# Kernel tuning notes

Measured on AMD Instinct MI355X. Metric: run time of the kernel, lower is better.

Reference implementation:

```python
import jax, jax.numpy as jnp
import numpy as np


def _made_masks(D, H):
    # Standard MADE masks, natural ordering, param_count=2 (shift, log_scale).
    d_in = np.arange(1, D + 1)                      # input degrees 1..D
    d_h = (np.arange(H) % (D - 1)) + 1              # hidden degrees cycle 1..D-1
    d_out = np.tile(d_in, 2)                        # output degrees, 2 params per dim
    M1 = (d_h[None, :] >= d_in[:, None]).astype(np.float32)   # [D, H]
    M2 = (d_out[None, :] > d_h[:, None]).astype(np.float32)
    return jnp.asarray(M1), jnp.asarray(M2)


def setup_inputs() -> dict:
    key = jax.random.key(0)
    B, D, H = 4096, 1024, 4096
    k0, k1, k2 = jax.random.split(key, 3)
    z = jax.random.normal(k0, (B, D), dtype=jnp.float32)
    W1 = jax.random.normal(k1, (D, H), dtype=jnp.float32) * (1.0 / np.sqrt(D))
    b1 = jnp.zeros((H,), dtype=jnp.float32)
    # small init on output layer keeps exp(log_scale) well-conditioned
    W2 = jax.random.normal(k2, (H, 2 * D), dtype=jnp.float32) * (0.1 / np.sqrt(H))
    b2 = jnp.zeros((2 * D,), dtype=jnp.float32)
    permutation = jnp.arange(D, dtype=jnp.int32)
    return {"z": z, "W1": W1, "b1": b1, "W2": W2, "b2": b2, "permutation": permutation}


def reference(z, W1, b1, W2, b2, permutation):
    # IAR.forward_flow: permute -> MADE masked MLP -> split params -> affine transform -> inverse permute
    D = z.shape[1]
    H = W1.shape[1]
    M1, M2 = _made_masks(D, H)
    zp = z[:, permutation]                          # permute_data
    h = jax.nn.relu(zp @ (W1 * M1) + b1)            # [B, H]
    res = h @ (W2 * M2) + b2                        # [B, 2D]
    mu, log_s = res[:, :D], res[:, D:]              # res.split(dim_in, dim=1)
    x = zp * jnp.exp(log_s) + mu                    # affine transform, forward=True
    log_det = jnp.sum(log_s, axis=1)                # [B]
    inv = jnp.argsort(permutation)                  # inv_permute_data
    return x[:, inv], log_det
```

## Files before the change

kernel.cpp:

```cpp
#include <hip/hip_runtime.h>
#include <stdint.h>


typedef float   f32x4  __attribute__((ext_vector_type(4)));
typedef int     i32x4  __attribute__((ext_vector_type(4)));
typedef int     i32x8  __attribute__((ext_vector_type(8)));

__device__ __forceinline__ uint8_t f2fp8(float f) {
    int p = __builtin_amdgcn_cvt_pk_fp8_f32(f, 0.0f, 0, false);
    return (uint8_t)(p & 0xff);
}
__device__ __forceinline__ int8_t f2i8(float v, float s) {
    float q = rintf(v * s);
    q = fminf(fmaxf(q, -127.0f), 127.0f);
    return (int8_t)q;
}

#define GLD16(g, l)                                                          \
    __builtin_amdgcn_global_load_lds(                                        \
        (const __attribute__((address_space(1))) uint32_t*)(g),              \
        (__attribute__((address_space(3))) uint32_t*)(l), 16, 0, 0)

#define MFMA_MX(a, b, c)                                                     \
    __builtin_amdgcn_mfma_scale_f32_16x16x128_f8f6f4(                        \
        (a), (b), (c), 0, 0, 0, 0x7F7F7F7F, 0, 0x7F7F7F7F)

__global__ __launch_bounds__(256) void mt1_k(
    const float* __restrict__ W, int8_t* __restrict__ WT, int R, int C, int Dv,
    float* __restrict__ ld, float* __restrict__ ws2, int B) {
    __shared__ int8_t t[64][68];
    const int c0 = blockIdx.x * 64, r0 = blockIdx.y * 64;
    const int tid = threadIdx.x;
    const int tx = tid & 63, ty = tid >> 6;

    const int fid = (blockIdx.y * gridDim.x + blockIdx.x) * 256 + tid;
    if (fid < B) ld[fid] = 0.0f;
    else if (fid < B + C) ws2[fid - B] = 0.0f;

    for (int rr = ty; rr < 64; rr += 4) {
        const int r = r0 + rr, c = c0 + tx;
        float v = W[(size_t)r * C + c];
        t[rr][tx] = ((c % (Dv - 1)) >= r) ? f2i8(v, 1024.0f) : (int8_t)0;
    }
    __syncthreads();
#pragma unroll
    for (int pass = 0; pass < 2; pass++) {
        const int cc = pass * 32 + (tid >> 3);
        const int j0 = (tid & 7) * 8;
        union { int8_t b[8]; uint64_t q; } v;
#pragma unroll
        for (int j = 0; j < 8; j++) v.b[j] = t[j0 + j][cc];
        *(uint64_t*)&WT[(size_t)(c0 + cc) * R + r0 + j0] = v.q;
    }
}

__global__ __launch_bounds__(256) void mt2_k(
    const float* __restrict__ W, uint8_t* __restrict__ WT,
    float* __restrict__ ws2, int R, int C, int Dv) {
    __shared__ uint8_t t[64][68];
    const int c0 = blockIdx.x * 64, r0 = blockIdx.y * 64;
    const int tid = threadIdx.x;
    const int tx = tid & 63, ty = tid >> 6;
    const bool second = (c0 >= Dv);
    for (int rr = ty; rr < 64; rr += 4) {
        const int r = r0 + rr, c = c0 + tx;
        float v = W[(size_t)r * C + c];
        bool keep = ((c % Dv) > (r % (Dv - 1)));
        t[rr][tx] = keep ? f2fp8(v * 256.0f) : (uint8_t)0;
        if (second) {
            float s = keep ? v : 0.0f;
#pragma unroll
            for (int o = 32; o > 0; o >>= 1) s += __shfl_down(s, o, 64);
            if (tx == 0) atomicAdd(&ws2[r], s);
        }
    }
    __syncthreads();
#pragma unroll
    for (int pass = 0; pass < 2; pass++) {
        const int cc = pass * 32 + (tid >> 3);
        const int j0 = (tid & 7) * 8;
        union { uint8_t b[8]; uint64_t q; } v;
#pragma unroll
        for (int j = 0; j < 8; j++) v.b[j] = t[j0 + j][cc];
        *(uint64_t*)&WT[(size_t)(c0 + cc) * R + r0 + j0] = v.q;
    }
}

__global__ __launch_bounds__(256) void perm_k(
    const float* __restrict__ z, const int* __restrict__ perm,
    int8_t* __restrict__ zp, int D) {
    const int b = blockIdx.y;
    const int i = blockIdx.x * 256 + threadIdx.x;
    zp[(size_t)b * D + i] = f2i8(z[(size_t)b * D + perm[i]], 32.0f);
}

__global__ __launch_bounds__(256) void gemm1_k(
    const int8_t* __restrict__ A, const int8_t* __restrict__ Bt,
    const float* __restrict__ bias, const float* __restrict__ wsum2,
    uint8_t* __restrict__ Cout, float* __restrict__ ld,
    int M, int N, int K) {
    __shared__ __align__(16) int8_t Alds[128 * 128];
    __shared__ __align__(16) int8_t Blds[128 * 128];
    __shared__ float pdl[128];

    const int id   = blockIdx.x;
    const int xcd  = id & 7, s = id >> 3;
    const int mb   = s & 31;
    const int nb   = xcd * 4 + (s >> 5);
    const int m0   = mb * 128;
    const int n0   = nb * 128;

    const int tid  = threadIdx.x;
    const int lane = tid & 63;
    const int w    = tid >> 6;
    const int wm   = (w & 1) * 64;
    const int wn   = (w >> 1) * 64;
    const int quad = lane >> 4;
    const int l16  = lane & 15;

    i32x4 acc[4][4];
#pragma unroll
    for (int i = 0; i < 4; i++)
#pragma unroll
        for (int j = 0; j < 4; j++) acc[i][j] = (i32x4)0;

    const int8_t* Ag[4];
    const int8_t* Bg[4];
    int8_t *Al[4], *Bl[4];
#pragma unroll
    for (int k = 0; k < 4; k++) {
        const int c  = tid + k * 256;
        const int so = ((c & 7) ^ ((c >> 3) & 7)) * 16;
        Ag[k] = A + (size_t)(m0 + (c >> 3)) * K + so;
        Bg[k] = Bt + (size_t)(n0 + (c >> 3)) * K + so;
        Al[k] = &Alds[c * 16];
        Bl[k] = &Blds[c * 16];
    }

    const int sw   = l16 & 7;
    const int arow = (wm + l16) * 128;
    const int brow = (wn + l16) * 128;

    for (int kt = 0; kt < K; kt += 128) {
        __syncthreads();
#pragma unroll
        for (int k = 0; k < 4; k++) {
            GLD16(Ag[k] + kt, Al[k]);
            GLD16(Bg[k] + kt, Bl[k]);
        }
        __syncthreads();

#pragma unroll
        for (int kh = 0; kh < 2; kh++) {
            const int pc = ((kh * 4 + quad) ^ sw) * 16;
            i32x4 af[4], bfr[4];
#pragma unroll
            for (int mi = 0; mi < 4; mi++)
                af[mi] = *(const i32x4*)&Alds[arow + mi * 16 * 128 + pc];
#pragma unroll
            for (int ni = 0; ni < 4; ni++)
                bfr[ni] = *(const i32x4*)&Blds[brow + ni * 16 * 128 + pc];
#pragma unroll
            for (int mi = 0; mi < 4; mi++)
#pragma unroll
                for (int ni = 0; ni < 4; ni++)
                    acc[mi][ni] = __builtin_amdgcn_mfma_i32_16x16x64_i8(
                        af[mi], bfr[ni], acc[mi][ni], 0, 0, 0);
        }
    }

    const float inv = 1.0f / 32768.0f;
    float bv[4], wv[4];
#pragma unroll
    for (int ni = 0; ni < 4; ni++) {
        bv[ni] = bias[n0 + wn + ni * 16 + l16];
        wv[ni] = wsum2[n0 + wn + ni * 16 + l16];
    }
    float pd[4][4];
#pragma unroll
    for (int mi = 0; mi < 4; mi++)
#pragma unroll
        for (int r = 0; r < 4; r++) pd[mi][r] = 0.0f;

#pragma unroll
    for (int mi = 0; mi < 4; mi++) {
        const int row = m0 + wm + mi * 16 + quad * 4;
#pragma unroll
        for (int ni = 0; ni < 4; ni++) {
            const int col = n0 + wn + ni * 16 + l16;
#pragma unroll
            for (int r = 0; r < 4; r++) {
                float v = fmaxf((float)acc[mi][ni][r] * inv + bv[ni], 0.0f);
                pd[mi][r] += v * wv[ni];
                Cout[(size_t)(row + r) * N + col] = f2fp8(v);
            }
        }
    }

#pragma unroll
    for (int off = 1; off < 16; off <<= 1)
#pragma unroll
        for (int mi = 0; mi < 4; mi++)
#pragma unroll
            for (int r = 0; r < 4; r++)
                pd[mi][r] += __shfl_xor(pd[mi][r], off, 16);

    __syncthreads();
    if ((w >> 1) == 0 && l16 == 0)
#pragma unroll
        for (int mi = 0; mi < 4; mi++)
#pragma unroll
            for (int r = 0; r < 4; r++)
                pdl[wm + mi * 16 + quad * 4 + r] = pd[mi][r];
    __syncthreads();
    if ((w >> 1) == 1 && l16 == 0)
#pragma unroll
        for (int mi = 0; mi < 4; mi++)
#pragma unroll
            for (int r = 0; r < 4; r++)
                pdl[wm + mi * 16 + quad * 4 + r] += pd[mi][r];
    __syncthreads();
    if (tid < 128) atomicAdd(&ld[m0 + tid], pdl[tid]);
}

__global__ __launch_bounds__(256) void gemm2f_k(
    const uint8_t* __restrict__ A, const uint8_t* __restrict__ Bt,
    const float* __restrict__ b2, const int* __restrict__ perm,
    const float* __restrict__ z, const float* __restrict__ ld,
    float* __restrict__ out, int B, int D, int K) {
    __shared__ __align__(16) uint8_t Alds[64 * 128];
    __shared__ __align__(16) uint8_t Blds[256 * 128];
    __shared__ float red[4];

    const int id   = blockIdx.x;
    const int nb   = id & 7;
    const int s    = id >> 3;
    const int m0   = s * 64;
    const int n0   = nb * 128;

    const int tid  = threadIdx.x;
    const int lane = tid & 63;
    const int w    = tid >> 6;
    const int wm   = (w & 1) * 32;
    const int wn   = (w >> 1) * 64;
    const int quad = lane >> 4;
    const int l16  = lane & 15;

    f32x4 acc[2][8];
#pragma unroll
    for (int i = 0; i < 2; i++)
#pragma unroll
        for (int j = 0; j < 8; j++) acc[i][j] = (f32x4)0.0f;

    const uint8_t* Ag[2];
    uint8_t* Al[2];
#pragma unroll
    for (int k = 0; k < 2; k++) {
        const int c  = tid + k * 256;
        const int so = ((c & 7) ^ ((c >> 3) & 7)) * 16;
        Ag[k] = A + (size_t)(m0 + (c >> 3)) * K + so;
        Al[k] = &Alds[c * 16];
    }
    const uint8_t* Bg[8];
    uint8_t* Bl[8];
#pragma unroll
    for (int k = 0; k < 8; k++) {
        const int c  = tid + k * 256;
        const int r  = c >> 3;
        const int g  = (r < 128) ? (n0 + r) : (D + n0 + (r - 128));
        const int so = ((c & 7) ^ (r & 7)) * 16;
        Bg[k] = Bt + (size_t)g * K + so;
        Bl[k] = &Blds[c * 16];
    }

    const int sw   = l16 & 7;
    const int pc0  = ((quad * 2) ^ sw) * 16;
    const int pc1  = ((quad * 2 + 1) ^ sw) * 16;
    const int arow = (wm + l16) * 128;
    int brow[8];
#pragma unroll
    for (int ni = 0; ni < 8; ni++)
        brow[ni] = ((ni >> 2) * 128 + wn + (ni & 3) * 16 + l16) * 128;

    for (int kt = 0; kt < K; kt += 128) {
        __syncthreads();
#pragma unroll
        for (int k = 0; k < 2; k++) GLD16(Ag[k] + kt, Al[k]);
#pragma unroll
        for (int k = 0; k < 8; k++) GLD16(Bg[k] + kt, Bl[k]);
        __syncthreads();

        union AB { int4 h2[2]; i32x8 v; };
        i32x8 af[2], bfr[8];
#pragma unroll
        for (int mi = 0; mi < 2; mi++) {
            AB t;
            t.h2[0] = *(const int4*)&Alds[arow + mi * 16 * 128 + pc0];
            t.h2[1] = *(const int4*)&Alds[arow + mi * 16 * 128 + pc1];
            af[mi] = t.v;
        }
#pragma unroll
        for (int ni = 0; ni < 8; ni++) {
            AB t;
            t.h2[0] = *(const int4*)&Blds[brow[ni] + pc0];
            t.h2[1] = *(const int4*)&Blds[brow[ni] + pc1];
            bfr[ni] = t.v;
        }
#pragma unroll
        for (int mi = 0; mi < 2; mi++)
#pragma unroll
            for (int ni = 0; ni < 8; ni++)
                acc[mi][ni] = MFMA_MX(af[mi], bfr[ni], acc[mi][ni]);
    }

    const float inv = 1.0f / 256.0f;
    float bmu[4], bls[4];
    int   pcv[4];
#pragma unroll
    for (int ci = 0; ci < 4; ci++) {
        const int gc = n0 + wn + ci * 16 + l16;
        bmu[ci] = b2[gc];
        bls[ci] = b2[D + gc];
        pcv[ci] = perm[gc];
    }
#pragma unroll
    for (int mi = 0; mi < 2; mi++) {
        const int row0 = m0 + wm + mi * 16 + quad * 4;
#pragma unroll
        for (int ci = 0; ci < 4; ci++) {
#pragma unroll
            for (int r = 0; r < 4; r++) {
                const size_t idx = (size_t)(row0 + r) * D + pcv[ci];
                const float mu = acc[mi][ci][r] * inv + bmu[ci];
                float ls = acc[mi][ci + 4][r] * inv + bls[ci];
                ls = fminf(fmaxf(ls, -30.0f), 30.0f);
                out[idx] = z[idx] * expf(ls) + mu;
            }
        }
    }

    if (nb == 0) {
        float bs = 0.0f;
        for (int i = tid; i < D; i += 256) bs += b2[D + i];
#pragma unroll
        for (int o = 32; o > 0; o >>= 1) bs += __shfl_down(bs, o, 64);
        if ((tid & 63) == 0) red[tid >> 6] = bs;
        __syncthreads();
        if (tid < 64)
            out[(size_t)B * D + m0 + tid] =
                ld[m0 + tid] + red[0] + red[1] + red[2] + red[3];
    }
}

extern "C" void kernel_launch(void* const* d_in, const int* in_sizes, int n_in,
                              void* d_out, int out_size, void* d_ws, size_t ws_size,
                              hipStream_t stream) {
    const float* z    = (const float*)d_in[0];
    const float* W1   = (const float*)d_in[1];
    const float* b1   = (const float*)d_in[2];
    const float* W2   = (const float*)d_in[3];
    const float* b2   = (const float*)d_in[4];
    const int*   perm = (const int*)d_in[5];
    float* out = (float*)d_out;
    char*  ws  = (char*)d_ws;

    const int D = in_sizes[5];
    const int H = in_sizes[2];
    const int B = in_sizes[0] / D;

    const size_t off_h    = 0;
    const size_t off_W2mT = off_h    + (size_t)B * H;
    const size_t off_W1mT = off_W2mT + (size_t)2 * D * H;
    const size_t off_zp   = off_W1mT + (size_t)H * D;
    const size_t off_ws2  = off_zp   + (size_t)B * D;
    const size_t off_ld   = off_ws2  + (size_t)H * 4;

    uint8_t* h    = (uint8_t*)(ws + off_h);
    uint8_t* W2mT = (uint8_t*)(ws + off_W2mT);
    int8_t*  W1mT = (int8_t*)(ws + off_W1mT);
    int8_t*  zp   = (int8_t*)(ws + off_zp);
    float*   ws2  = (float*)(ws + off_ws2);
    float*   ld   = (float*)(ws + off_ld);

    mt1_k<<<dim3(H / 64, D / 64), 256, 0, stream>>>(W1, W1mT, D, H, D, ld, ws2, B);
    mt2_k<<<dim3(2 * D / 64, H / 64), 256, 0, stream>>>(W2, W2mT, ws2, H, 2 * D, D);
    perm_k<<<dim3(D / 256, B), 256, 0, stream>>>(z, perm, zp, D);

    gemm1_k<<<(H / 128) * (B / 128), 256, 0, stream>>>(
        zp, W1mT, b1, ws2, h, ld, B, H, D);

    gemm2f_k<<<(D / 128) * (B / 64), 256, 0, stream>>>(
        h, W2mT, b2, perm, z, ld, out, B, D, H);
}
```

Measured before the change: 207.4 us.

## Fuse weight-mask transposes and permute into one prep kernel with partial sums

Merges the three preprocessing kernels (W1 mask/quantize/transpose, W2 mask/quantize/transpose, permute+quantize of z) into a single launch with block-range dispatch. The atomicAdd-based row-sum of the masked log-scale weights becomes per-column-block partial sums written to a 16xH buffer, which gemm1's epilogue sums itself, so the zero-init of that buffer goes away. The permute path now handles four elements and two rows per thread with vectorized perm loads and packed stores. This cuts launch overhead and atomic contention, at the cost of 16 extra loads per column in the gemm1 epilogue.

```diff
diff --git a/kernel.cpp b/kernel.cpp
--- a/kernel.cpp
+++ b/kernel.cpp
@@ -25,78 +25,94 @@
     __builtin_amdgcn_mfma_scale_f32_16x16x128_f8f6f4(                        \
         (a), (b), (c), 0, 0, 0, 0x7F7F7F7F, 0, 0x7F7F7F7F)
 
-__global__ __launch_bounds__(256) void mt1_k(
-    const float* __restrict__ W, int8_t* __restrict__ WT, int R, int C, int Dv,
-    float* __restrict__ ld, float* __restrict__ ws2, int B) {
-    __shared__ int8_t t[64][68];
-    const int c0 = blockIdx.x * 64, r0 = blockIdx.y * 64;
+__global__ __launch_bounds__(256) void prep_k(
+    const float* __restrict__ W1, int8_t* __restrict__ W1mT,
+    const float* __restrict__ W2, uint8_t* __restrict__ W2mT,
+    float* __restrict__ ws2p,
+    const float* __restrict__ z, const int* __restrict__ perm,
+    int8_t* __restrict__ zp, float* __restrict__ ld,
+    int D, int H, int B) {
+    const int bx  = blockIdx.x;
     const int tid = threadIdx.x;
-    const int tx = tid & 63, ty = tid >> 6;
-
-    const int fid = (blockIdx.y * gridDim.x + blockIdx.x) * 256 + tid;
-    if (fid < B) ld[fid] = 0.0f;
-    else if (fid < B + C) ws2[fid - B] = 0.0f;
-
-    for (int rr = ty; rr < 64; rr += 4) {
-        const int r = r0 + rr, c = c0 + tx;
-        float v = W[(size_t)r * C + c];
-        t[rr][tx] = ((c % (Dv - 1)) >= r) ? f2i8(v, 1024.0f) : (int8_t)0;
-    }
-    __syncthreads();
-#pragma unroll
-    for (int pass = 0; pass < 2; pass++) {
-        const int cc = pass * 32 + (tid >> 3);
-        const int j0 = (tid & 7) * 8;
-        union { int8_t b[8]; uint64_t q; } v;
-#pragma unroll
-        for (int j = 0; j < 8; j++) v.b[j] = t[j0 + j][cc];
-        *(uint64_t*)&WT[(size_t)(c0 + cc) * R + r0 + j0] = v.q;
-    }
-}
-
-__global__ __launch_bounds__(256) void mt2_k(
-    const float* __restrict__ W, uint8_t* __restrict__ WT,
-    float* __restrict__ ws2, int R, int C, int Dv) {
-    __shared__ uint8_t t[64][68];
-    const int c0 = blockIdx.x * 64, r0 = blockIdx.y * 64;
-    const int tid = threadIdx.x;
-    const int tx = tid & 63, ty = tid >> 6;
-    const bool second = (c0 >= Dv);
-    for (int rr = ty; rr < 64; rr += 4) {
-        const int r = r0 + rr, c = c0 + tx;
-        float v = W[(size_t)r * C + c];
-        bool keep = ((c % Dv) > (r % (Dv - 1)));
-        t[rr][tx] = keep ? f2fp8(v * 256.0f) : (uint8_t)0;
-        if (second) {
-            float s = keep ? v : 0.0f;
-#pragma unroll
-            for (int o = 32; o > 0; o >>= 1) s += __shfl_down(s, o, 64);
-            if (tx == 0) atomicAdd(&ws2[r], s);
-        }
-    }
-    __syncthreads();
-#pragma unroll
-    for (int pass = 0; pass < 2; pass++) {
-        const int cc = pass * 32 + (tid >> 3);
-        const int j0 = (tid & 7) * 8;
-        union { uint8_t b[8]; uint64_t q; } v;
-#pragma unroll
-        for (int j = 0; j < 8; j++) v.b[j] = t[j0 + j][cc];
-        *(uint64_t*)&WT[(size_t)(c0 + cc) * R + r0 + j0] = v.q;
-    }
-}
-
-__global__ __launch_bounds__(256) void perm_k(
-    const float* __restrict__ z, const int* __restrict__ perm,
-    int8_t* __restrict__ zp, int D) {
-    const int b = blockIdx.y;
-    const int i = blockIdx.x * 256 + threadIdx.x;
-    zp[(size_t)b * D + i] = f2i8(z[(size_t)b * D + perm[i]], 32.0f);
+    const int NB1 = (H / 64) * (D / 64);
+    const int NB2 = (2 * D / 64) * (H / 64);
+
+    if (bx < NB1) {
+        __shared__ int8_t t[64][68];
+        const int c0 = (bx % (H / 64)) * 64;
+        const int r0 = (bx / (H / 64)) * 64;
+        const int tx = tid & 63, ty = tid >> 6;
+
+        const int fid = bx * 256 + tid;
+        if (fid < B) ld[fid] = 0.0f;
+
+        for (int rr = ty; rr < 64; rr += 4) {
+            const int r = r0 + rr, c = c0 + tx;
+            float v = W1[(size_t)r * H + c];
+            t[rr][tx] = ((c % (D - 1)) >= r) ? f2i8(v, 1024.0f) : (int8_t)0;
+        }
+        __syncthreads();
+#pragma unroll
+        for (int pass = 0; pass < 2; pass++) {
+            const int cc = pass * 32 + (tid >> 3);
+            const int j0 = (tid & 7) * 8;
+            union { int8_t b[8]; uint64_t q; } v;
+#pragma unroll
+            for (int j = 0; j < 8; j++) v.b[j] = t[j0 + j][cc];
+            *(uint64_t*)&W1mT[(size_t)(c0 + cc) * D + r0 + j0] = v.q;
+        }
+    } else if (bx < NB1 + NB2) {
+        __shared__ uint8_t t[64][68];
+        const int idx = bx - NB1;
+        const int c0 = (idx % (2 * D / 64)) * 64;
+        const int r0 = (idx / (2 * D / 64)) * 64;
+        const int tx = tid & 63, ty = tid >> 6;
+        const bool second = (c0 >= D);
+        const int cb = (c0 - D) >> 6;
+
+        for (int rr = ty; rr < 64; rr += 4) {
+            const int r = r0 + rr, c = c0 + tx;
+            float v = W2[(size_t)r * 2 * D + c];
+            bool keep = ((c % D) > (r % (D - 1)));
+            t[rr][tx] = keep ? f2fp8(v * 256.0f) : (uint8_t)0;
+            if (second) {
+                float s = keep ? v : 0.0f;
+#pragma unroll
+                for (int o = 32; o > 0; o >>= 1) s += __shfl_down(s, o, 64);
+                if (tx == 0) ws2p[(size_t)cb * H + r] = s;
+            }
+        }
+        __syncthreads();
+#pragma unroll
+        for (int pass = 0; pass < 2; pass++) {
+            const int cc = pass * 32 + (tid >> 3);
+            const int j0 = (tid & 7) * 8;
+            union { uint8_t b[8]; uint64_t q; } v;
+#pragma unroll
+            for (int j = 0; j < 8; j++) v.b[j] = t[j0 + j][cc];
+            *(uint64_t*)&W2mT[(size_t)(c0 + cc) * H + r0 + j0] = v.q;
+        }
+    } else {
+        const int bp = bx - NB1 - NB2;
+        const int i0 = tid * 4;
+        const int4 p4 = *(const int4*)(perm + i0);
+#pragma unroll
+        for (int rr = 0; rr < 2; rr++) {
+            const int b = bp * 2 + rr;
+            const float* zr = z + (size_t)b * D;
+            union { int8_t b4[4]; uint32_t u; } q;
+            q.b4[0] = f2i8(zr[p4.x], 32.0f);
+            q.b4[1] = f2i8(zr[p4.y], 32.0f);
+            q.b4[2] = f2i8(zr[p4.z], 32.0f);
+            q.b4[3] = f2i8(zr[p4.w], 32.0f);
+            *(uint32_t*)&zp[(size_t)b * D + i0] = q.u;
+        }
+    }
 }
 
 __global__ __launch_bounds__(256) void gemm1_k(
     const int8_t* __restrict__ A, const int8_t* __restrict__ Bt,
-    const float* __restrict__ bias, const float* __restrict__ wsum2,
+    const float* __restrict__ bias, const float* __restrict__ ws2p,
     uint8_t* __restrict__ Cout, float* __restrict__ ld,
     int M, int N, int K) {
     __shared__ __align__(16) int8_t Alds[128 * 128];
@@ -173,8 +189,12 @@
     float bv[4], wv[4];
 #pragma unroll
     for (int ni = 0; ni < 4; ni++) {
-        bv[ni] = bias[n0 + wn + ni * 16 + l16];
-        wv[ni] = wsum2[n0 + wn + ni * 16 + l16];
+        const int col = n0 + wn + ni * 16 + l16;
+        bv[ni] = bias[col];
+        float sv = 0.0f;
+#pragma unroll
+        for (int cb = 0; cb < 16; cb++) sv += ws2p[(size_t)cb * N + col];
+        wv[ni] = sv;
     }
     float pd[4][4];
 #pragma unroll
@@ -373,21 +393,23 @@
     const size_t off_W1mT = off_W2mT + (size_t)2 * D * H;
     const size_t off_zp   = off_W1mT + (size_t)H * D;
     const size_t off_ws2  = off_zp   + (size_t)B * D;
-    const size_t off_ld   = off_ws2  + (size_t)H * 4;
+    const size_t off_ld   = off_ws2  + (size_t)16 * H * 4;
 
     uint8_t* h    = (uint8_t*)(ws + off_h);
     uint8_t* W2mT = (uint8_t*)(ws + off_W2mT);
     int8_t*  W1mT = (int8_t*)(ws + off_W1mT);
     int8_t*  zp   = (int8_t*)(ws + off_zp);
-    float*   ws2  = (float*)(ws + off_ws2);
+    float*   ws2p = (float*)(ws + off_ws2);
     float*   ld   = (float*)(ws + off_ld);
 
-    mt1_k<<<dim3(H / 64, D / 64), 256, 0, stream>>>(W1, W1mT, D, H, D, ld, ws2, B);
-    mt2_k<<<dim3(2 * D / 64, H / 64), 256, 0, stream>>>(W2, W2mT, ws2, H, 2 * D, D);
-    perm_k<<<dim3(D / 256, B), 256, 0, stream>>>(z, perm, zp, D);
+    const int NB1 = (H / 64) * (D / 64);
+    const int NB2 = (2 * D / 64) * (H / 64);
+    const int NBP = B / 2;
+    prep_k<<<NB1 + NB2 + NBP, 256, 0, stream>>>(
+        W1, W1mT, W2, W2mT, ws2p, z, perm, zp, ld, D, H, B);
 
     gemm1_k<<<(H / 128) * (B / 128), 256, 0, stream>>>(
-        zp, W1mT, b1, ws2, h, ld, B, H, D);
+        zp, W1mT, b1, ws2p, h, ld, B, H, D);
 
     gemm2f_k<<<(D / 128) * (B / 64), 256, 0, stream>>>(
         h, W2mT, b2, perm, z, ld, out, B, D, H);
```

Measured after the change: 194.4 us. 6.3% less time.
